# Optimization experiments

Measured on AMD Instinct MI355X. Metric: run time of the kernel, lower is better.

The kernel has to match this reference:

```python
import jax, jax.numpy as jnp
import numpy as np

N_WAY = 5
K_SHOT = 5
SEQ = 196          # patch tokens per image (ViT-S/16 @ 224)
TEMP = 0.0510310363  # similarity temperature ~ 1/sqrt(384)
LR = 0.1
OPT_STEPS = 15


def _normalize(emb):
    # [B, S, D] -> [B*S, D], rows L2-normalized with 1e-8 floor (matches torch.max(norm, 1e-8))
    v = emb.reshape(-1, emb.shape[-1])
    n = jnp.linalg.norm(v, axis=1, keepdims=True)
    return v / jnp.maximum(n, 1e-8)


def _block_mask():
    # block_diag of (SEQ x SEQ) blocks of -100 for each of the n_way*k_shot support images
    return jnp.kron(jnp.eye(N_WAY * K_SHOT, dtype=jnp.float32),
                    jnp.ones((SEQ, SEQ), jnp.float32)) * (-100.0)


def _predict(sup, qry, v, mask):
    # sup: [n_way*k_shot, S, D], qry: [Qb, Qs, D], v: [n_way*k_shot*S]
    S = sup.shape[1]
    Qb, Qs = qry.shape[0], qry.shape[1]
    C = _normalize(sup) @ _normalize(qry).T           # [Ls, Qb*Qs] cosine sims
    if mask is not None:
        C = C + mask
    pred = C + v[:, None]
    pred = pred.reshape(N_WAY, K_SHOT * S, Qb, Qs)
    pred = pred.transpose(0, 1, 3, 2).reshape(N_WAY, K_SHOT * S * Qs, Qb)
    pred = pred / TEMP
    pred = jax.scipy.special.logsumexp(pred, axis=1)  # [n_way, Qb]
    return pred.T                                     # [Qb, n_way]


def _optimize_v(sup_key, sup_query, labels, mask):
    # online SGD on the patch-embedding importance vector v (starts at zero)
    Ls = N_WAY * K_SHOT * sup_key.shape[1]
    B = sup_query.shape[0]

    def loss(v):
        p = _predict(sup_key, sup_query, v, mask)  # [B, n_way]
        logp = jax.nn.log_softmax(p, axis=1)
        return -jnp.mean(logp[jnp.arange(B), labels])

    def step(v, _):
        return v - LR * jax.grad(loss)(v), None

    v, _ = jax.lax.scan(step, jnp.zeros((Ls,), jnp.float32), None, length=OPT_STEPS)
    return v


def setup_inputs() -> dict:
    key = jax.random.key(0)
    k1, k2, k3, k4 = jax.random.split(key, 4)
    return {
        "support_emb_key": jax.random.normal(k1, (N_WAY * K_SHOT, SEQ, 384), jnp.float32),
        "support_emb_query": jax.random.normal(k2, (N_WAY * K_SHOT, SEQ, 384), jnp.float32),
        "query_emb": jax.random.normal(k3, (75, SEQ, 384), jnp.float32),
        "support_labels": jax.random.randint(k4, (N_WAY * K_SHOT,), 0, N_WAY, dtype=jnp.int32),
    }


def reference(support_emb_key, support_emb_query, query_emb, support_labels):
    mask = _block_mask()
    v = _optimize_v(support_emb_key, support_emb_query, support_labels, mask)
    return _predict(support_emb_key, query_emb, v, None)  # [75, n_way]
```

## Files before the change

kernel.cpp:

```cpp
#include <hip/hip_runtime.h>
#include <hip/hip_bf16.h>

#define NW 5
#define KS 5
#define SEQ 196
#define DIM 384
#define NSUP 25
#define NQRY 75
#define NIMG 100
#define LSUP 4900
#define LSUP_PAD 4992
#define QROWS 208
#define BLOCK_W 980
#define OPT_STEPS 15
#define MTILES 39

static constexpr float TEMP_F = 0.0510310363f;
static constexpr float INV_T  = 1.0f / TEMP_F;
static constexpr float LR_F   = 0.1f;

typedef short v8s __attribute__((ext_vector_type(8)));
typedef float v4f __attribute__((ext_vector_type(4)));

__device__ inline unsigned short f2bf(float x) {
    unsigned int u = __float_as_uint(x);
    u += 0x7fffu + ((u >> 16) & 1u);
    return (unsigned short)(u >> 16);
}

__global__ __launch_bounds__(256) void norm_all(const float* __restrict__ supk,
                                                const float* __restrict__ supq,
                                                const float* __restrict__ qry,
                                                unsigned short* __restrict__ Kb,
                                                unsigned short* __restrict__ Qall) {
    int R = blockIdx.x * 4 + (threadIdx.x >> 6);
    int l = threadIdx.x & 63;
    unsigned short* out;
    const float* in;
    float scale;
    if (R < LSUP_PAD) {
        out = Kb + (size_t)R * DIM;
        if (R >= LSUP) {
            #pragma unroll
            for (int k = 0; k < 6; ++k) out[l + 64 * k] = 0;
            return;
        }
        in = supk + (size_t)R * DIM;
        scale = INV_T;
    } else {
        int i = R - LSUP_PAD;
        int img = i / QROWS;
        int r = i - img * QROWS;
        out = Qall + (size_t)i * DIM;
        if (r >= SEQ) {
            #pragma unroll
            for (int k = 0; k < 6; ++k) out[l + 64 * k] = 0;
            return;
        }
        in = (img < NSUP)
            ? supq + ((size_t)img * SEQ + r) * DIM
            : qry  + ((size_t)(img - NSUP) * SEQ + r) * DIM;
        scale = 1.0f;
    }
    float x[6];
    #pragma unroll
    for (int k = 0; k < 6; ++k) x[k] = in[l + 64 * k];
    float s = 0.f;
    #pragma unroll
    for (int k = 0; k < 6; ++k) s += x[k] * x[k];
    #pragma unroll
    for (int m = 1; m < 64; m <<= 1) s += __shfl_xor(s, m);
    float sc = scale / fmaxf(sqrtf(s), 1e-8f);
    #pragma unroll
    for (int k = 0; k < 6; ++k) out[l + 64 * k] = f2bf(x[k] * sc);
}

#define MT  128
#define NTP 208
#define KCC 64

__device__ __forceinline__ void gload16(const void* g, void* l) {
    __builtin_amdgcn_global_load_lds(
        (__attribute__((address_space(1))) void*)g,
        (__attribute__((address_space(3))) void*)l, 16, 0, 0);
}

template<int IMG_BASE, int NWG>
__device__ __forceinline__ void gemm_body(
    int gid,
    const unsigned short* __restrict__ Kb,
    const unsigned short* __restrict__ Qall,
    float* __restrict__ Rall,
    unsigned short* Asm, unsigned short* Bsm)
{
    int t = threadIdx.x;

    constexpr int qq = NWG >> 3;
    constexpr int rr = NWG & 7;
    int xcd = gid & 7;
    int sub = gid >> 3;
    int L = (xcd < rr ? xcd * (qq + 1) : rr * (qq + 1) + (xcd - rr) * qq) + sub;
    int img = IMG_BASE + L / MTILES;
    int m_base = (L % MTILES) * MT;

    const unsigned short* Qimg = Qall + (size_t)img * (QROWS * DIM);

    int wv = t >> 6;
    int l  = t & 63;
    int lo = l & 15;
    int hi = l >> 4;
    int mh = (wv >> 1) * 64;
    int nh = wv & 1;

    int srow = l >> 3;
    int skp  = (l & 7) ^ srow;
    const unsigned short* aSrc = Kb   + (size_t)(m_base + wv * 32 + srow) * DIM + skp * 8;
    const unsigned short* bSrc = Qimg + (size_t)srow * DIM + skp * 8;

    v4f acc[4][7];
    #pragma unroll
    for (int m = 0; m < 4; ++m)
        #pragma unroll
        for (int n = 0; n < 7; ++n)
            acc[m][n] = (v4f){0.f, 0.f, 0.f, 0.f};

    for (int kb = 0; kb < DIM; kb += KCC) {
        #pragma unroll
        for (int j = 0; j < 4; ++j)
            gload16(aSrc + (size_t)j * 8 * DIM + kb,
                    Asm + (wv * 32 + j * 8) * KCC);
        #pragma unroll
        for (int jj = 0; jj < 7; ++jj) {
            int j = wv + jj * 4;
            if (j < 26)
                gload16(bSrc + (size_t)j * 8 * DIM + kb,
                        Bsm + j * 8 * KCC);
        }
        __syncthreads();

        const unsigned short* Ar = Asm + (mh + lo) * KCC;
        const unsigned short* Br = Bsm + (nh * 112 + lo) * KCC;
        #pragma unroll
        for (int kk = 0; kk < 2; ++kk) {
            int koff = ((hi + 4 * kk) ^ (lo & 7)) * 8;
            v8s a0 = *(const v8s*)(Ar + koff);
            v8s a1 = *(const v8s*)(Ar + 16 * KCC + koff);
            v8s a2 = *(const v8s*)(Ar + 32 * KCC + koff);
            v8s a3 = *(const v8s*)(Ar + 48 * KCC + koff);
            #pragma unroll
            for (int n = 0; n < 7; ++n) {
                if (nh == 0 || n < 6) {
                    v8s bb = *(const v8s*)(Br + n * 16 * KCC + koff);
                    acc[0][n] = __builtin_amdgcn_mfma_f32_16x16x32_bf16(a0, bb, acc[0][n], 0, 0, 0);
                    acc[1][n] = __builtin_amdgcn_mfma_f32_16x16x32_bf16(a1, bb, acc[1][n], 0, 0, 0);
                    acc[2][n] = __builtin_amdgcn_mfma_f32_16x16x32_bf16(a2, bb, acc[2][n], 0, 0, 0);
                    acc[3][n] = __builtin_amdgcn_mfma_f32_16x16x32_bf16(a3, bb, acc[3][n], 0, 0, 0);
                }
            }
        }
        __syncthreads();
    }

    float s[4][4];
    #pragma unroll
    for (int m = 0; m < 4; ++m)
        #pragma unroll
        for (int j = 0; j < 4; ++j) s[m][j] = 0.f;
    #pragma unroll
    for (int n = 0; n < 7; ++n) {
        if (nh == 0 || n < 6) {
            bool ok = ((nh * 7 + n) * 16 + lo) < SEQ;
            #pragma unroll
            for (int m = 0; m < 4; ++m)
                #pragma unroll
                for (int j = 0; j < 4; ++j)
                    s[m][j] += ok ? __expf(acc[m][n][j]) : 0.f;
        }
    }
    #pragma unroll
    for (int mm = 1; mm < 16; mm <<= 1) {
        #pragma unroll
        for (int m = 0; m < 4; ++m)
            #pragma unroll
            for (int j = 0; j < 4; ++j)
                s[m][j] += __shfl_xor(s[m][j], mm);
    }
    float* rp = (float*)Asm;
    if (lo == 0) {
        #pragma unroll
        for (int m = 0; m < 4; ++m)
            #pragma unroll
            for (int j = 0; j < 4; ++j)
                rp[nh * 128 + mh + m * 16 + hi * 4 + j] = s[m][j];
    }
    __syncthreads();
    if (t < MT) {
        int gr = m_base + t;
        if (gr < LSUP) {
            float o = rp[t] + rp[128 + t];
            if (img < NSUP && (gr / SEQ) == img) o = 0.f;
            Rall[(size_t)img * LSUP + gr] = o;
        }
    }
}

__global__ __launch_bounds__(256, 3) void gemm_support(
    const unsigned short* __restrict__ Kb,
    const unsigned short* __restrict__ Qall,
    float* __restrict__ Rall)
{
    __shared__ __align__(16) unsigned short Asm[MT * KCC];
    __shared__ __align__(16) unsigned short Bsm[NTP * KCC];
    gemm_body<0, NSUP * MTILES>(blockIdx.x, Kb, Qall, Rall, Asm, Bsm);
}

__global__ __launch_bounds__(256, 3) void mega(
    const unsigned short* __restrict__ Kb,
    const unsigned short* __restrict__ Qall,
    float* __restrict__ Rall,
    const int* __restrict__ labels,
    float* __restrict__ Dbufs,
    int* __restrict__ flags,
    float* __restrict__ e_out)
{
    __shared__ __align__(16) unsigned short Asm[MT * KCC];
    __shared__ __align__(16) unsigned short Bsm[NTP * KCC];

    if (blockIdx.x >= NW) {
        gemm_body<NSUP, NQRY * MTILES>((int)blockIdx.x - NW, Kb, Qall, Rall, Asm, Bsm);
        return;
    }

    float* sh  = (float*)Asm;
    float* red = sh;
    float* cfs = sh + 100;
    float* Dsm = sh + 128;
    int*   lsm = (int*)(sh + 256);

    int w = blockIdx.x;
    int t = threadIdx.x;
    int wave = t >> 6, lane = t & 63;

    float Rv[4][NSUP];
    #pragma unroll
    for (int b = 0; b < NSUP; ++b) {
        const float* Rb = Rall + (size_t)b * LSUP + w * BLOCK_W;
        Rv[0][b] = Rb[t];
        Rv[1][b] = Rb[t + 256];
        Rv[2][b] = Rb[t + 512];
        Rv[3][b] = (t < BLOCK_W - 768) ? Rb[t + 768] : 0.f;
    }
    if (t < NSUP) lsm[t] = labels[t];

    float e0 = 1.f, e1 = 1.f, e2 = 1.f, e3 = 1.f;
    float v0 = 0.f, v1 = 0.f, v2 = 0.f, v3 = 0.f;

    auto pushD = [&](int step) {
        float part[NSUP];
        #pragma unroll
        for (int b = 0; b < NSUP; ++b)
            part[b] = e0 * Rv[0][b] + e1 * Rv[1][b] + e2 * Rv[2][b] + e3 * Rv[3][b];
        #pragma unroll
        for (int b = 0; b < NSUP; ++b) {
            #pragma unroll
            for (int m = 32; m; m >>= 1) part[b] += __shfl_xor(part[b], m);
        }
        if (lane == 0) {
            #pragma unroll
            for (int b = 0; b < NSUP; ++b) red[wave * NSUP + b] = part[b];
        }
        __syncthreads();
        if (t < NSUP) {
            float s = red[t] + red[NSUP + t] + red[2 * NSUP + t] + red[3 * NSUP + t];
            __hip_atomic_store(&Dbufs[step * 125 + t * 5 + w], s,
                               __ATOMIC_RELAXED, __HIP_MEMORY_SCOPE_AGENT);
        }
        __syncthreads();
        if (t == 0)
            __hip_atomic_store(&flags[w], step + 1,
                               __ATOMIC_RELAXED, __HIP_MEMORY_SCOPE_AGENT);
    };

    pushD(0);

    for (int s = 0; s < OPT_STEPS; ++s) {
        if (wave == 0) {
            for (;;) {
                int f = (lane < NW)
                    ? __hip_atomic_load(&flags[lane], __ATOMIC_RELAXED, __HIP_MEMORY_SCOPE_AGENT)
                    : 0x7fffffff;
                if (__all(f >= s + 1)) break;
                __builtin_amdgcn_s_sleep(1);
            }
        }
        __syncthreads();
        if (t < 125)
            Dsm[t] = __hip_atomic_load(&Dbufs[s * 125 + t],
                                       __ATOMIC_RELAXED, __HIP_MEMORY_SCOPE_AGENT);
        __syncthreads();
        if (t < NSUP) {
            float Dsum = 0.f, Dw = 1.f;
            #pragma unroll
            for (int ww = 0; ww < NW; ++ww) {
                float d = Dsm[t * 5 + ww];
                Dsum += d;
                if (ww == w) Dw = d;
            }
            cfs[t] = ((Dw / Dsum) - (w == lsm[t] ? 1.f : 0.f)) * (INV_T / 25.f) / Dw;
        }
        __syncthreads();
        float g0 = 0.f, g1 = 0.f, g2 = 0.f, g3 = 0.f;
        #pragma unroll
        for (int b = 0; b < NSUP; ++b) {
            float c = cfs[b];
            g0 += c * Rv[0][b];
            g1 += c * Rv[1][b];
            g2 += c * Rv[2][b];
            g3 += c * Rv[3][b];
        }
        v0 -= LR_F * e0 * g0; e0 = __expf(v0 * INV_T);
        v1 -= LR_F * e1 * g1; e1 = __expf(v1 * INV_T);
        v2 -= LR_F * e2 * g2; e2 = __expf(v2 * INV_T);
        v3 -= LR_F * e3 * g3; e3 = __expf(v3 * INV_T);
        __syncthreads();
        if (s + 1 < OPT_STEPS) pushD(s + 1);
    }

    float* eo = e_out + w * BLOCK_W;
    eo[t]       = e0;
    eo[t + 256] = e1;
    eo[t + 512] = e2;
    if (t < BLOCK_W - 768) eo[t + 768] = e3;
}

__global__ __launch_bounds__(256) void final_pred(const float* __restrict__ Rall,
                                                  const float* __restrict__ e_out,
                                                  float* __restrict__ out) {
    __shared__ float ws[4];
    int blk = blockIdx.x;
    int qb = blk / 5, w = blk % 5;
    const float* R  = Rall + (size_t)(NSUP + qb) * LSUP + w * BLOCK_W;
    const float* eb = e_out + w * BLOCK_W;
    int t = threadIdx.x;
    float p = 0.f;
    for (int i = t; i < BLOCK_W; i += 256) p += eb[i] * R[i];
    #pragma unroll
    for (int m = 32; m; m >>= 1) p += __shfl_xor(p, m);
    if ((t & 63) == 0) ws[t >> 6] = p;
    __syncthreads();
    if (t == 0) out[blk] = logf(ws[0] + ws[1] + ws[2] + ws[3]);
}

extern "C" void kernel_launch(void* const* d_in, const int* in_sizes, int n_in,
                              void* d_out, int out_size, void* d_ws, size_t ws_size,
                              hipStream_t stream) {
    const float* sup_key = (const float*)d_in[0];
    const float* sup_qry = (const float*)d_in[1];
    const float* qry     = (const float*)d_in[2];
    const int*   labels  = (const int*)d_in[3];
    float* out = (float*)d_out;

    char* ws = (char*)d_ws;
    size_t off = 0;
    auto take = [&](size_t bytes) {
        char* p = ws + off;
        off = (off + bytes + 255) & ~(size_t)255;
        return p;
    };
    unsigned short* Kb   = (unsigned short*)take((size_t)LSUP_PAD * DIM * 2);
    unsigned short* Qall = (unsigned short*)take((size_t)NIMG * QROWS * DIM * 2);
    float*          Rall = (float*)take((size_t)NIMG * LSUP * 4);
    float*          Dbuf = (float*)take(((size_t)(OPT_STEPS + 1) * 125 + 32) * 4);
    float*          eout = (float*)take((size_t)LSUP * 4);
    int*            flags = (int*)(Dbuf + (OPT_STEPS + 1) * 125);

    hipMemsetAsync(Dbuf, 0, ((size_t)(OPT_STEPS + 1) * 125 + 32) * 4, stream);

    norm_all<<<(LSUP_PAD + NIMG * QROWS) / 4, 256, 0, stream>>>(
        sup_key, sup_qry, qry, Kb, Qall);

    gemm_support<<<NSUP * MTILES, 256, 0, stream>>>(Kb, Qall, Rall);

    mega<<<NW + NQRY * MTILES, 256, 0, stream>>>(Kb, Qall, Rall, labels, Dbuf, flags, eout);

    final_pred<<<NQRY * NW, 256, 0, stream>>>(Rall, eout, out);
}
```

Baseline: 219.8 us.

## Fold support GEMM into mega kernel with atomic completion counter

Removes the separate support-GEMM launch and runs those tiles inside the mega kernel. The optimizer blocks spin on a global done counter until every support tile has been written, then start the SGD loop while the query GEMM tiles run alongside. Flag and buffer polling now uses atomic fetch-add of zero so each read sees fresh values, and the sleep intervals are lengthened. This saves one launch boundary and overlaps the tail of the support GEMM with the query GEMM. The spin-wait depends on the low block indices being scheduled before, or alongside, the support blocks they wait on.

```diff
diff --git a/kernel.cpp b/kernel.cpp
--- a/kernel.cpp
+++ b/kernel.cpp
@@ -14,6 +14,8 @@
 #define BLOCK_W 980
 #define OPT_STEPS 15
 #define MTILES 39
+#define NSUPWG (NSUP * MTILES)
+#define NQWG   (NQRY * MTILES)
 
 static constexpr float TEMP_F = 0.0510310363f;
 static constexpr float INV_T  = 1.0f / TEMP_F;
@@ -26,6 +28,16 @@
     unsigned int u = __float_as_uint(x);
     u += 0x7fffu + ((u >> 16) & 1u);
     return (unsigned short)(u >> 16);
+}
+
+__device__ __forceinline__ float fresh_f32(float* p) {
+    return __hip_atomic_fetch_add(p, 0.0f, __ATOMIC_RELAXED, __HIP_MEMORY_SCOPE_AGENT);
+}
+__device__ __forceinline__ int fresh_i32(int* p) {
+    return __hip_atomic_fetch_add(p, 0, __ATOMIC_RELAXED, __HIP_MEMORY_SCOPE_AGENT);
+}
+__device__ __forceinline__ unsigned fresh_u32(unsigned* p) {
+    return __hip_atomic_fetch_add(p, 0u, __ATOMIC_RELAXED, __HIP_MEMORY_SCOPE_AGENT);
 }
 
 __global__ __launch_bounds__(256) void norm_all(const float* __restrict__ supk,
@@ -85,12 +97,13 @@
         (__attribute__((address_space(3))) void*)l, 16, 0, 0);
 }
 
-template<int IMG_BASE, int NWG>
+template<int IMG_BASE, int NWG, bool SUPPORT>
 __device__ __forceinline__ void gemm_body(
     int gid,
     const unsigned short* __restrict__ Kb,
     const unsigned short* __restrict__ Qall,
     float* __restrict__ Rall,
+    unsigned* done,
     unsigned short* Asm, unsigned short* Bsm)
 {
     int t = threadIdx.x;
@@ -199,19 +212,18 @@
         if (gr < LSUP) {
             float o = rp[t] + rp[128 + t];
             if (img < NSUP && (gr / SEQ) == img) o = 0.f;
-            Rall[(size_t)img * LSUP + gr] = o;
-        }
-    }
-}
-
-__global__ __launch_bounds__(256, 3) void gemm_support(
-    const unsigned short* __restrict__ Kb,
-    const unsigned short* __restrict__ Qall,
-    float* __restrict__ Rall)
-{
-    __shared__ __align__(16) unsigned short Asm[MT * KCC];
-    __shared__ __align__(16) unsigned short Bsm[NTP * KCC];
-    gemm_body<0, NSUP * MTILES>(blockIdx.x, Kb, Qall, Rall, Asm, Bsm);
+            if (SUPPORT)
+                __hip_atomic_store(&Rall[(size_t)img * LSUP + gr], o,
+                                   __ATOMIC_RELAXED, __HIP_MEMORY_SCOPE_AGENT);
+            else
+                Rall[(size_t)img * LSUP + gr] = o;
+        }
+    }
+    if (SUPPORT) {
+        __syncthreads();
+        if (t == 0)
+            __hip_atomic_fetch_add(done, 1u, __ATOMIC_RELAXED, __HIP_MEMORY_SCOPE_AGENT);
+    }
 }
 
 __global__ __launch_bounds__(256, 3) void mega(
@@ -221,13 +233,20 @@
     const int* __restrict__ labels,
     float* __restrict__ Dbufs,
     int* __restrict__ flags,
+    unsigned* __restrict__ done,
     float* __restrict__ e_out)
 {
     __shared__ __align__(16) unsigned short Asm[MT * KCC];
     __shared__ __align__(16) unsigned short Bsm[NTP * KCC];
 
+    if (blockIdx.x >= NW + NSUPWG) {
+        gemm_body<NSUP, NQWG, false>((int)blockIdx.x - (NW + NSUPWG),
+                                     Kb, Qall, Rall, done, Asm, Bsm);
+        return;
+    }
     if (blockIdx.x >= NW) {
-        gemm_body<NSUP, NQRY * MTILES>((int)blockIdx.x - NW, Kb, Qall, Rall, Asm, Bsm);
+        gemm_body<0, NSUPWG, true>((int)blockIdx.x - NW,
+                                   Kb, Qall, Rall, done, Asm, Bsm);
         return;
     }
 
@@ -240,6 +259,12 @@
     int w = blockIdx.x;
     int t = threadIdx.x;
     int wave = t >> 6, lane = t & 63;
+
+    if (t == 0) {
+        while (fresh_u32(done) < (unsigned)NSUPWG)
+            __builtin_amdgcn_s_sleep(8);
+    }
+    __syncthreads();
 
     float Rv[4][NSUP];
     #pragma unroll
@@ -286,17 +311,14 @@
     for (int s = 0; s < OPT_STEPS; ++s) {
         if (wave == 0) {
             for (;;) {
-                int f = (lane < NW)
-                    ? __hip_atomic_load(&flags[lane], __ATOMIC_RELAXED, __HIP_MEMORY_SCOPE_AGENT)
-                    : 0x7fffffff;
+                int f = (lane < NW) ? fresh_i32(&flags[lane]) : 0x7fffffff;
                 if (__all(f >= s + 1)) break;
-                __builtin_amdgcn_s_sleep(1);
+                __builtin_amdgcn_s_sleep(4);
             }
         }
         __syncthreads();
         if (t < 125)
-            Dsm[t] = __hip_atomic_load(&Dbufs[s * 125 + t],
-                                       __ATOMIC_RELAXED, __HIP_MEMORY_SCOPE_AGENT);
+            Dsm[t] = fresh_f32(&Dbufs[s * 125 + t]);
         __syncthreads();
         if (t < NSUP) {
             float Dsum = 0.f, Dw = 1.f;
@@ -370,18 +392,18 @@
     unsigned short* Kb   = (unsigned short*)take((size_t)LSUP_PAD * DIM * 2);
     unsigned short* Qall = (unsigned short*)take((size_t)NIMG * QROWS * DIM * 2);
     float*          Rall = (float*)take((size_t)NIMG * LSUP * 4);
-    float*          Dbuf = (float*)take(((size_t)(OPT_STEPS + 1) * 125 + 32) * 4);
+    float*          Dbuf = (float*)take(((size_t)(OPT_STEPS + 1) * 125 + 64) * 4);
     float*          eout = (float*)take((size_t)LSUP * 4);
     int*            flags = (int*)(Dbuf + (OPT_STEPS + 1) * 125);
-
-    hipMemsetAsync(Dbuf, 0, ((size_t)(OPT_STEPS + 1) * 125 + 32) * 4, stream);
+    unsigned*       done  = (unsigned*)(flags + 8);
+
+    hipMemsetAsync(Dbuf, 0, ((size_t)(OPT_STEPS + 1) * 125 + 64) * 4, stream);
 
     norm_all<<<(LSUP_PAD + NIMG * QROWS) / 4, 256, 0, stream>>>(
         sup_key, sup_qry, qry, Kb, Qall);
 
-    gemm_support<<<NSUP * MTILES, 256, 0, stream>>>(Kb, Qall, Rall);
-
-    mega<<<NW + NQRY * MTILES, 256, 0, stream>>>(Kb, Qall, Rall, labels, Dbuf, flags, eout);
+    mega<<<NW + NSUPWG + NQWG, 256, 0, stream>>>(
+        Kb, Qall, Rall, labels, Dbuf, flags, done, eout);
 
     final_pred<<<NQRY * NW, 256, 0, stream>>>(Rall, eout, out);
 }
```

After: 219.6 us. About the same (-0.1%).
